# Kernel tuning notes

Measured on AMD Instinct MI355X. Metric: run time of the kernel, lower is better.

## Reference

```python
import jax, jax.numpy as jnp
import numpy as np

B, S, D = 1, 2048, 2048
H = 16
HD = D // H           # 128
FFN_H = 5632          # int(2*4*D/3) rounded up to multiple of 256
EPS = 1e-5
ROPE_THETA = 10000.0


def rms_norm(x, w, eps=EPS):
    # x * rsqrt(mean(x^2, -1) + eps) * w
    return x * jax.lax.rsqrt(jnp.mean(x * x, axis=-1, keepdims=True) + eps) * w


def apply_rope(x, cos, sin):
    # x: [B, S, H, HD]; cos/sin: [S, HD//2]
    b, s, h, hd = x.shape
    xr = x.reshape(b, s, h, hd // 2, 2)
    x_re, x_im = xr[..., 0], xr[..., 1]
    c = cos[None, :, None, :]
    sn = sin[None, :, None, :]
    o_re = x_re * c - x_im * sn
    o_im = x_re * sn + x_im * c
    return jnp.stack([o_re, o_im], axis=-1).reshape(b, s, h, hd)


def setup_inputs() -> dict:
    key = jax.random.key(0)
    ks = jax.random.split(key, 10)
    x = jax.random.normal(ks[0], (B, S, D), dtype=jnp.float32)
    # RoPE frequencies (Llama-style)
    inv_freq = 1.0 / (ROPE_THETA ** (np.arange(0, HD, 2, dtype=np.float32) / HD))
    angles = np.outer(np.arange(S, dtype=np.float32), inv_freq)  # [S, HD//2]
    freqs_cos = jnp.asarray(np.cos(angles), dtype=jnp.float32)
    freqs_sin = jnp.asarray(np.sin(angles), dtype=jnp.float32)
    # causal mask: 1 = keep, 0 = masked
    mask = jnp.tril(jnp.ones((S, S), dtype=jnp.int32))[None, None]
    sc = 0.02
    return {
        "x": x,
        "freqs_cos": freqs_cos,
        "freqs_sin": freqs_sin,
        "mask": mask,
        "wq": jax.random.normal(ks[1], (D, D), jnp.float32) * sc,
        "wk": jax.random.normal(ks[2], (D, D), jnp.float32) * sc,
        "wv": jax.random.normal(ks[3], (D, D), jnp.float32) * sc,
        "wo": jax.random.normal(ks[4], (D, D), jnp.float32) * sc,
        "w1": jax.random.normal(ks[5], (D, FFN_H), jnp.float32) * sc,
        "w2": jax.random.normal(ks[6], (FFN_H, D), jnp.float32) * sc,
        "w3": jax.random.normal(ks[7], (D, FFN_H), jnp.float32) * sc,
        "attn_norm_w": jnp.ones((D,), jnp.float32),
        "ffn_norm_w": jnp.ones((D,), jnp.float32),
    }


def reference(x, freqs_cos, freqs_sin, mask, wq, wk, wv, wo, w1, w2, w3,
              attn_norm_w, ffn_norm_w):
    b, s, d = x.shape
    # --- attention block ---
    xn = rms_norm(x, attn_norm_w)
    q = (xn @ wq).reshape(b, s, H, HD)
    k = (xn @ wk).reshape(b, s, H, HD)
    v = (xn @ wv).reshape(b, s, H, HD)
    q = apply_rope(q, freqs_cos, freqs_sin)
    k = apply_rope(k, freqs_cos, freqs_sin)
    scores = jnp.einsum('bqhd,bkhd->bhqk', q, k) / jnp.sqrt(jnp.float32(HD))
    scores = jnp.where(mask == 0, -jnp.inf, scores)
    probs = jax.nn.softmax(scores, axis=-1)
    attn = jnp.einsum('bhqk,bkhd->bqhd', probs, v).reshape(b, s, d)
    h = x + attn @ wo
    # --- SwiGLU FFN block ---
    hn = rms_norm(h, ffn_norm_w)
    ff = (jax.nn.silu(hn @ w1) * (hn @ w3)) @ w2
    return h + ff
```

## Files before the change

kernel.cpp:

```cpp
#include <hip/hip_runtime.h>
#include <hip/hip_bf16.h>

typedef __bf16 bf16x8 __attribute__((ext_vector_type(8)));
typedef float f32x4 __attribute__((ext_vector_type(4)));
typedef unsigned short u16x8 __attribute__((ext_vector_type(8)));
typedef unsigned short u16x4 __attribute__((ext_vector_type(4)));

#define DEV static __device__ __forceinline__

DEV unsigned short f2bf(float f) {
    unsigned u = __builtin_bit_cast(unsigned, f);
    u += 0x7fffu + ((u >> 16) & 1u);
    return (unsigned short)(u >> 16);
}
DEV float bf2f(unsigned short h) {
    unsigned u = ((unsigned)h) << 16;
    return __builtin_bit_cast(float, u);
}

DEV void gl2lds16(const void* g, void* l) {
    __builtin_amdgcn_global_load_lds(
        (const __attribute__((address_space(1))) void*)g,
        (__attribute__((address_space(3))) void*)l, 16, 0, 0);
}

#define WAITV(N) asm volatile("s_waitcnt vmcnt(" #N ")" ::: "memory")
#define SBAR()   asm volatile("s_barrier" ::: "memory")

#define STAGE128D(KT, BUF)                                                    \
    _Pragma("unroll")                                                         \
    for (int sl = 0; sl < 3; ++sl) {                                          \
        const unsigned short* sbase = (sl == 0)                               \
            ? A  + (size_t)bm * K                                             \
            : BT + (size_t)(bn + (sl - 1) * 128) * K;                         \
        _Pragma("unroll")                                                     \
        for (int j = 0; j < 2; ++j) {                                         \
            const unsigned short* g = sbase + (size_t)(srow + j * 64) * K     \
                                      + koff + (KT) * 64 + lc;                \
            gl2lds16(g, &lds[BUF][sl][wave * 512 + j * 4096]);                \
        }                                                                     \
    }

#define DSREAD128(BUF)                                                        \
    {                                                                         \
        const char* Ab = (const char*)&lds[BUF][0][0];                        \
        const char* Bb = (const char*)&lds[BUF][1 + (wn >> 1)][0];            \
        _Pragma("unroll")                                                     \
        for (int m4 = 0; m4 < 4; ++m4)                                        \
            _Pragma("unroll")                                                 \
            for (int kk = 0; kk < 2; ++kk)                                    \
                a_[m4][kk] = *(const bf16x8*)(Ab +                            \
                    (wm * 64 + m4 * 16 + lr) * 128 +                          \
                    ((kk * 64 + lg * 16) ^ xsw));                             \
        _Pragma("unroll")                                                     \
        for (int n2 = 0; n2 < 4; ++n2)                                        \
            _Pragma("unroll")                                                 \
            for (int kk = 0; kk < 2; ++kk)                                    \
                b_[n2][kk] = *(const bf16x8*)(Bb +                            \
                    ((wn & 1) * 64 + n2 * 16 + lr) * 128 +                    \
                    ((kk * 64 + lg * 16) ^ xsw));                             \
    }

#define MFMA128                                                               \
    __builtin_amdgcn_s_setprio(1);                                            \
    _Pragma("unroll")                                                         \
    for (int m4 = 0; m4 < 4; ++m4)                                            \
        _Pragma("unroll")                                                     \
        for (int n2 = 0; n2 < 4; ++n2)                                        \
            _Pragma("unroll")                                                 \
            for (int kk = 0; kk < 2; ++kk)                                    \
                acc[m4][n2] = __builtin_amdgcn_mfma_f32_16x16x32_bf16(        \
                    a_[m4][kk], b_[n2][kk], acc[m4][n2], 0, 0, 0);            \
    __builtin_amdgcn_s_setprio(0);

template <int EPI>
__global__ __launch_bounds__(512, 2)
void gemm128d(const unsigned short* __restrict__ A,
              const unsigned short* __restrict__ BT,
              unsigned short* __restrict__ outB,
              float* __restrict__ outP,
              int M, int N, int K,
              const float* __restrict__ cs, const float* __restrict__ sn,
              unsigned short* __restrict__ vT)
{
    __shared__ alignas(16) unsigned short lds[3][3][8192];
    const int tid  = threadIdx.x;
    const int lane = tid & 63;
    const int wave = tid >> 6;
    const int wm = wave >> 2;
    const int wn = wave & 3;
    const int lr = lane & 15;
    const int lg = lane >> 4;
    const int gy  = gridDim.y;
    const int lin = blockIdx.y * gridDim.x + blockIdx.x;
    const int cpx = (gridDim.x * gy) >> 3;
    const int swz = (lin & 7) * cpx + (lin >> 3);
    const int bm = (swz % gy) * 128;
    const int bn = (swz / gy) * 256;
    const int xsw  = (lr & 7) << 4;
    const int srow = tid >> 3;
    const int lc   = ((tid & 7) ^ (srow & 7)) * 8;
    int koff, NT;
    if constexpr (EPI == 1 || EPI == 3) {
        const int Kh = K >> 1; koff = blockIdx.z * Kh; NT = Kh >> 6;
    } else {
        koff = 0; NT = K >> 6;
    }

    f32x4 acc[4][4] = {};
    bf16x8 a_[4][2], b_[4][2];

    STAGE128D(0, 0);
    STAGE128D(1, 1);
    WAITV(6); SBAR();
    DSREAD128(0);

    int bc = 0;
    for (int kt = 0; kt < NT - 2; ++kt) {
        const int nb = (bc == 0) ? 2 : bc - 1;
        STAGE128D(kt + 2, nb);
        MFMA128;
        WAITV(6); SBAR();
        const int rb = (bc == 2) ? 0 : bc + 1;
        DSREAD128(rb);
        bc = rb;
    }
    MFMA128;
    WAITV(0); SBAR();
    {
        const int rb = (bc == 2) ? 0 : bc + 1;
        DSREAD128(rb);
    }
    MFMA128;

#pragma unroll
    for (int m4 = 0; m4 < 4; ++m4) {
        const int row = bm + wm * 64 + m4 * 16 + lg * 4;
#pragma unroll
        for (int n2 = 0; n2 < 4; ++n2) {
            const int col = bn + wn * 64 + n2 * 16 + lr;
            if constexpr (EPI == 4) {
                if (bn >= 4096) {
                    u16x4 o;
#pragma unroll
                    for (int r = 0; r < 4; ++r) o[r] = f2bf(acc[m4][n2][r]);
                    *(u16x4*)(vT + (size_t)(col - 4096) * 2048 + row) = o;
                } else {
#pragma unroll
                    for (int r = 0; r < 4; ++r) {
                        const float v  = acc[m4][n2][r];
                        const float vo = __shfl_xor(v, 1);
                        const int rr = row + r;
                        const int i0 = (col & 127) >> 1;
                        const float c = cs[rr * 64 + i0];
                        const float s = sn[rr * 64 + i0];
                        const float o = (lr & 1) ? (vo * s + v * c)
                                                 : (v * c - vo * s);
                        outB[(size_t)rr * N + col] = f2bf(o);
                    }
                }
            } else {
#pragma unroll
                for (int r = 0; r < 4; ++r) {
                    if constexpr (EPI == 1) {
                        outP[(size_t)blockIdx.z * M * N + (size_t)(row + r) * N + col] = acc[m4][n2][r];
                    } else if constexpr (EPI == 3) {
                        unsafeAtomicAdd(&outP[(size_t)(row + r) * N + col], acc[m4][n2][r]);
                    } else {
                        const float v  = acc[m4][n2][r];
                        const float vo = __shfl_xor(v, 1);
                        const float x1 = (lr & 1) ? vo : v;
                        const float x3 = (lr & 1) ? v : vo;
                        const float g  = x1 / (1.0f + __expf(-x1)) * x3;
                        if (!(lr & 1))
                            outB[(size_t)(row + r) * (N >> 1) + (col >> 1)] = f2bf(g);
                    }
                }
            }
        }
    }
}

__global__ __launch_bounds__(256)
void reduce2_norm(const float* __restrict__ res, const float* __restrict__ p,
                  const float* __restrict__ w, float* __restrict__ hout,
                  unsigned short* __restrict__ nout)
{
    const int row = blockIdx.x, tid = threadIdx.x;
    const float4* r4 = (const float4*)(res + (size_t)row * 2048);
    const float4* a4 = (const float4*)(p   + (size_t)row * 2048);
    const float4* b4 = (const float4*)(p + (size_t)2048 * 2048 + (size_t)row * 2048);
    float4* h4 = (float4*)(hout + (size_t)row * 2048);
    float4 h[2];
    float ss = 0.f;
#pragma unroll
    for (int i = 0; i < 2; ++i) {
        const int idx = i * 256 + tid;
        const float4 r = r4[idx], a = a4[idx], b = b4[idx];
        float4 v = make_float4(r.x + a.x + b.x, r.y + a.y + b.y,
                               r.z + a.z + b.z, r.w + a.w + b.w);
        h[i] = v; h4[idx] = v;
        ss += v.x * v.x + v.y * v.y + v.z * v.z + v.w * v.w;
    }
#pragma unroll
    for (int off = 32; off; off >>= 1) ss += __shfl_xor(ss, off);
    __shared__ float red[4];
    if ((tid & 63) == 0) red[tid >> 6] = ss;
    __syncthreads();
    const float tot = red[0] + red[1] + red[2] + red[3];
    const float sc = rsqrtf(tot * (1.0f / 2048.0f) + 1e-5f);
#pragma unroll
    for (int i = 0; i < 2; ++i) {
        const int idx = i * 256 + tid;
        const float4 wv = ((const float4*)w)[idx];
        u16x4 o;
        o[0] = f2bf(h[i].x * sc * wv.x); o[1] = f2bf(h[i].y * sc * wv.y);
        o[2] = f2bf(h[i].z * sc * wv.z); o[3] = f2bf(h[i].w * sc * wv.w);
        *(u16x4*)(nout + (size_t)row * 2048 + idx * 4) = o;
    }
}

__global__ __launch_bounds__(256)
void rmsnorm_kernel(const float* __restrict__ x, const float* __restrict__ w,
                    unsigned short* __restrict__ out)
{
    const int row = blockIdx.x;
    const int tid = threadIdx.x;
    const float* xr = x + (size_t)row * 2048;
    const float4 a = *reinterpret_cast<const float4*>(xr + tid * 8);
    const float4 b = *reinterpret_cast<const float4*>(xr + tid * 8 + 4);
    float ss = a.x * a.x + a.y * a.y + a.z * a.z + a.w * a.w
             + b.x * b.x + b.y * b.y + b.z * b.z + b.w * b.w;
#pragma unroll
    for (int off = 32; off; off >>= 1) ss += __shfl_xor(ss, off);
    __shared__ float red[4];
    if ((tid & 63) == 0) red[tid >> 6] = ss;
    __syncthreads();
    const float tot = red[0] + red[1] + red[2] + red[3];
    const float sc = rsqrtf(tot * (1.0f / 2048.0f) + 1e-5f);
    const float4 wa = *reinterpret_cast<const float4*>(w + tid * 8);
    const float4 wb = *reinterpret_cast<const float4*>(w + tid * 8 + 4);
    u16x8 o;
    o[0] = f2bf(a.x * sc * wa.x); o[1] = f2bf(a.y * sc * wa.y);
    o[2] = f2bf(a.z * sc * wa.z); o[3] = f2bf(a.w * sc * wa.w);
    o[4] = f2bf(b.x * sc * wb.x); o[5] = f2bf(b.y * sc * wb.y);
    o[6] = f2bf(b.z * sc * wb.z); o[7] = f2bf(b.w * sc * wb.w);
    *reinterpret_cast<u16x8*>(out + (size_t)row * 2048 + tid * 8) = o;
}

DEV void convT_body(const float* __restrict__ w, unsigned short* __restrict__ wT,
                    int K, int N, int rmul, int radd, int bk, int bn, int tid)
{
    __shared__ unsigned short t[64][66];
    const int r = tid >> 4, c4 = (tid & 15) * 4;
#pragma unroll
    for (int i = 0; i < 4; ++i) {
        const int row = r + i * 16;
        const float4 v = *reinterpret_cast<const float4*>(w + (size_t)(bk + row) * N + bn + c4);
        t[row][c4 + 0] = f2bf(v.x); t[row][c4 + 1] = f2bf(v.y);
        t[row][c4 + 2] = f2bf(v.z); t[row][c4 + 3] = f2bf(v.w);
    }
    __syncthreads();
#pragma unroll
    for (int i = 0; i < 4; ++i) {
        const int n = r + i * 16;
        u16x4 o;
#pragma unroll
        for (int e = 0; e < 4; ++e) o[e] = t[c4 + e][n];
        *reinterpret_cast<u16x4*>(wT + (size_t)(rmul * (bn + n) + radd) * K + bk + c4) = o;
    }
}

__global__ __launch_bounds__(256)
void convT_kernel(const float* __restrict__ w, unsigned short* __restrict__ wT,
                  int K, int N)
{
    convT_body(w, wT, K, N, 1, 0, blockIdx.y * 64, blockIdx.x * 64, threadIdx.x);
}

__global__ __launch_bounds__(256)
void convT4_kernel(const float* __restrict__ w0, const float* __restrict__ w1,
                   const float* __restrict__ w2, const float* __restrict__ w3,
                   unsigned short* __restrict__ wT)
{
    const int z = blockIdx.z;
    const float* w = (z == 0) ? w0 : (z == 1) ? w1 : (z == 2) ? w2 : w3;
    convT_body(w, wT + (size_t)z * 2048 * 2048, 2048, 2048, 1, 0,
               blockIdx.y * 64, blockIdx.x * 64, threadIdx.x);
}

__global__ __launch_bounds__(256)
void convTpair_kernel(const float* __restrict__ wa, const float* __restrict__ wb,
                      unsigned short* __restrict__ wT)
{
    const int z = blockIdx.z;
    convT_body(z ? wb : wa, wT, 2048, 5632, 2, z,
               blockIdx.y * 64, blockIdx.x * 64, threadIdx.x);
}

__global__ __launch_bounds__(512)
void flash_attn(const unsigned short* __restrict__ q,
                const unsigned short* __restrict__ k,
                const unsigned short* __restrict__ vT,
                unsigned short* __restrict__ attn)
{
    __shared__ alignas(16) unsigned short Ks[2][64][136];
    __shared__ alignas(16) unsigned short Vs[2][128][72];
    __shared__ alignas(16) unsigned short Ps[8][16][72];

    const int hh = blockIdx.y;
    const int pi = blockIdx.x;
    const int tid = threadIdx.x;
    const int lane = tid & 63, wave = tid >> 6;
    const int qt = (wave >> 2) ? (31 - pi) : pi;
    const int lr = lane & 15, lg = lane >> 4;
    const int q0 = qt * 64 + (wave & 3) * 16;
    const int myNT = qt + 1;
    const int NT   = 32 - pi;

    const int kr0 = tid >> 4, kc0 = (tid & 15) * 8;
    const int vr0 = tid >> 3, vc0 = (tid & 7) * 8;

    bf16x8 qf[4];
#pragma unroll
    for (int c = 0; c < 4; ++c)
        qf[c] = *reinterpret_cast<const bf16x8*>(
            q + (size_t)(q0 + lr) * 6144 + hh * 128 + c * 32 + lg * 8);

    f32x4 oacc[8] = {};
    float m_r[4], l_r[4];
#pragma unroll
    for (int r = 0; r < 4; ++r) { m_r[r] = -INFINITY; l_r[r] = 0.0f; }
    const float scale = 0.08838834764831845f;

    u16x8 kreg0, kreg1, vreg0, vreg1;
    auto gload = [&](int kt) {
        const int kv0 = kt * 64;
        kreg0 = *reinterpret_cast<const u16x8*>(k + (size_t)(kv0 + kr0) * 6144 + hh * 128 + kc0);
        kreg1 = *reinterpret_cast<const u16x8*>(k + (size_t)(kv0 + kr0 + 32) * 6144 + hh * 128 + kc0);
        vreg0 = *reinterpret_cast<const u16x8*>(vT + (size_t)(hh * 128 + vr0) * 2048 + kv0 + vc0);
        vreg1 = *reinterpret_cast<const u16x8*>(vT + (size_t)(hh * 128 + vr0 + 64) * 2048 + kv0 + vc0);
    };
    auto lwrite = [&](int buf) {
        *reinterpret_cast<u16x8*>(&Ks[buf][kr0][kc0])      = kreg0;
        *reinterpret_cast<u16x8*>(&Ks[buf][kr0 + 32][kc0]) = kreg1;
        *reinterpret_cast<u16x8*>(&Vs[buf][vr0][vc0])      = vreg0;
        *reinterpret_cast<u16x8*>(&Vs[buf][vr0 + 64][vc0]) = vreg1;
    };

    gload(0); lwrite(0);
    __syncthreads();

    for (int kt = 0; kt < NT; ++kt) {
        const int buf = kt & 1;
        if (kt + 1 < NT) gload(kt + 1);

        if (kt < myNT) {
            const int kv0 = kt * 64;
            const bool masked = (kt == myNT - 1);
            f32x4 s[4] = {};
            __builtin_amdgcn_s_setprio(1);
#pragma unroll
            for (int ct = 0; ct < 4; ++ct)
#pragma unroll
                for (int c = 0; c < 4; ++c) {
                    const bf16x8 kf = *reinterpret_cast<const bf16x8*>(
                        &Ks[buf][ct * 16 + lr][c * 32 + lg * 8]);
                    s[ct] = __builtin_amdgcn_mfma_f32_16x16x32_bf16(qf[c], kf, s[ct], 0, 0, 0);
                }
            __builtin_amdgcn_s_setprio(0);
#pragma unroll
            for (int ct = 0; ct < 4; ++ct)
#pragma unroll
                for (int r = 0; r < 4; ++r) {
                    float v = s[ct][r] * scale;
                    if (masked) {
                        const int kvg = kv0 + ct * 16 + lr;
                        const int qg  = q0 + lg * 4 + r;
                        if (kvg > qg) v = -INFINITY;
                    }
                    s[ct][r] = v;
                }
            float mn[4], alpha[4], rs[4];
#pragma unroll
            for (int r = 0; r < 4; ++r) {
                float v = fmaxf(fmaxf(s[0][r], s[1][r]), fmaxf(s[2][r], s[3][r]));
                v = fmaxf(v, __shfl_xor(v, 1));
                v = fmaxf(v, __shfl_xor(v, 2));
                v = fmaxf(v, __shfl_xor(v, 4));
                v = fmaxf(v, __shfl_xor(v, 8));
                mn[r] = fmaxf(m_r[r], v);
                alpha[r] = __expf(m_r[r] - mn[r]);
                m_r[r] = mn[r];
                rs[r] = 0.0f;
            }
#pragma unroll
            for (int ct = 0; ct < 4; ++ct)
#pragma unroll
                for (int r = 0; r < 4; ++r) {
                    const float p = __expf(s[ct][r] - mn[r]);
                    s[ct][r] = p;
                    rs[r] += p;
                }
#pragma unroll
            for (int r = 0; r < 4; ++r) {
                float t2 = rs[r];
                t2 += __shfl_xor(t2, 1);
                t2 += __shfl_xor(t2, 2);
                t2 += __shfl_xor(t2, 4);
                t2 += __shfl_xor(t2, 8);
                l_r[r] = l_r[r] * alpha[r] + t2;
            }
#pragma unroll
            for (int ot = 0; ot < 8; ++ot)
#pragma unroll
                for (int r = 0; r < 4; ++r) oacc[ot][r] *= alpha[r];

#pragma unroll
            for (int ct = 0; ct < 4; ++ct)
#pragma unroll
                for (int r = 0; r < 4; ++r)
                    Ps[wave][lg * 4 + r][ct * 16 + lr] = f2bf(s[ct][r]);

            __builtin_amdgcn_s_setprio(1);
#pragma unroll
            for (int c2 = 0; c2 < 2; ++c2) {
                const bf16x8 pf = *reinterpret_cast<const bf16x8*>(
                    &Ps[wave][lr][c2 * 32 + lg * 8]);
#pragma unroll
                for (int ot = 0; ot < 8; ++ot) {
                    const bf16x8 vf = *reinterpret_cast<const bf16x8*>(
                        &Vs[buf][ot * 16 + lr][c2 * 32 + lg * 8]);
                    oacc[ot] = __builtin_amdgcn_mfma_f32_16x16x32_bf16(pf, vf, oacc[ot], 0, 0, 0);
                }
            }
            __builtin_amdgcn_s_setprio(0);
        }

        if (kt + 1 < NT) lwrite(buf ^ 1);
        __syncthreads();
    }

#pragma unroll
    for (int ot = 0; ot < 8; ++ot)
#pragma unroll
        for (int r = 0; r < 4; ++r) {
            const float v = oacc[ot][r] / l_r[r];
            attn[(size_t)(q0 + lg * 4 + r) * 2048 + hh * 128 + ot * 16 + lr] = f2bf(v);
        }
}

extern "C" void kernel_launch(void* const* d_in, const int* in_sizes, int n_in,
                              void* d_out, int out_size, void* d_ws, size_t ws_size,
                              hipStream_t stream)
{
    const float* x    = (const float*)d_in[0];
    const float* fcos = (const float*)d_in[1];
    const float* fsin = (const float*)d_in[2];
    const float* wq  = (const float*)d_in[4];
    const float* wk  = (const float*)d_in[5];
    const float* wv  = (const float*)d_in[6];
    const float* wo  = (const float*)d_in[7];
    const float* w1  = (const float*)d_in[8];
    const float* w2  = (const float*)d_in[9];
    const float* w3  = (const float*)d_in[10];
    const float* anw = (const float*)d_in[11];
    const float* fnw = (const float*)d_in[12];
    float* out = (float*)d_out;

    char* ws = (char*)d_ws;
    size_t off = 0;
    auto alloc = [&](size_t bytes) { void* p = ws + off; off += bytes; return p; };
    const size_t SZ_DD = (size_t)2048 * 2048 * 2;
    const size_t SZ_DF = (size_t)2048 * 5632 * 2;

    unsigned short* qkvoT = (unsigned short*)alloc(4 * SZ_DD);
    unsigned short* w13T  = (unsigned short*)alloc(2 * SZ_DF);
    unsigned short* w2T   = (unsigned short*)alloc(SZ_DF);

    char* reg1 = (char*)alloc((size_t)48 * 1024 * 1024);
    unsigned short* xn   = (unsigned short*)reg1;
    unsigned short* qkv  = (unsigned short*)(reg1 + SZ_DD);
    unsigned short* vTb  = (unsigned short*)(reg1 + SZ_DD + 3 * SZ_DD);
    unsigned short* ab   = (unsigned short*)(reg1 + SZ_DD + 4 * SZ_DD);
    float*          pk   = (float*)reg1;
    unsigned short* hn   = (unsigned short*)(reg1 + 4 * SZ_DD);

    char* reg2 = (char*)alloc(SZ_DF);
    unsigned short* t1 = (unsigned short*)reg2;

    convT4_kernel<<<dim3(32, 32, 4), 256, 0, stream>>>(wq, wk, wv, wo, qkvoT);
    convTpair_kernel<<<dim3(88, 32, 2), 256, 0, stream>>>(w1, w3, w13T);
    convT_kernel<<<dim3(32, 88), 256, 0, stream>>>(w2, w2T, 5632, 2048);

    rmsnorm_kernel<<<2048, 256, 0, stream>>>(x, anw, xn);
    gemm128d<4><<<dim3(24, 16), 512, 0, stream>>>(xn, qkvoT, qkv, nullptr,
                                                  2048, 6144, 2048, fcos, fsin, vTb);
    flash_attn<<<dim3(16, 16), 512, 0, stream>>>(qkv, qkv + 2048, vTb, ab);
    gemm128d<1><<<dim3(8, 16, 2), 512, 0, stream>>>(ab, qkvoT + 3 * (size_t)2048 * 2048,
                                                    nullptr, pk, 2048, 2048, 2048,
                                                    nullptr, nullptr, nullptr);
    reduce2_norm<<<2048, 256, 0, stream>>>(x, pk, fnw, out, hn);

    gemm128d<2><<<dim3(44, 16), 512, 0, stream>>>(hn, w13T, t1, nullptr,
                                                  2048, 11264, 2048,
                                                  nullptr, nullptr, nullptr);
    gemm128d<3><<<dim3(8, 16, 2), 512, 0, stream>>>(t1, w2T, nullptr, out,
                                                    2048, 2048, 5632,
                                                    nullptr, nullptr, nullptr);
}
```

Measured before the change: 432.2 us.

## Fold wo/w1/w3/w2 weight conversion into flash-attention launch as extra blocks

Only the wq/wk/wv transposes stay in front of the QKV GEMM. The wo, w1/w3 and w2 fp32-to-bf16 transposes now run as extra blocks (256 and up) in the flash attention launch, each 512-thread block doing two 64x64 tiles. Attention uses only 256 blocks, so the conversion work can fill otherwise idle CUs and overlap with attention instead of running serially. The cost is a larger LDS footprint per block, which may lower attention occupancy, and the scheduler may mix or order conversion blocks poorly alongside the attention blocks.

```diff
diff --git a/kernel.cpp b/kernel.cpp
--- a/kernel.cpp
+++ b/kernel.cpp
@@ -248,10 +248,10 @@
     *reinterpret_cast<u16x8*>(out + (size_t)row * 2048 + tid * 8) = o;
 }
 
-DEV void convT_body(const float* __restrict__ w, unsigned short* __restrict__ wT,
-                    int K, int N, int rmul, int radd, int bk, int bn, int tid)
-{
-    __shared__ unsigned short t[64][66];
+DEV void convT_half(const float* __restrict__ w, unsigned short* __restrict__ wT,
+                    int K, int N, int rmul, int radd, int bk, int bn,
+                    int tid, unsigned short (*t)[66])
+{
     const int r = tid >> 4, c4 = (tid & 15) * 4;
 #pragma unroll
     for (int i = 0; i < 4; ++i) {
@@ -272,45 +272,58 @@
 }
 
 __global__ __launch_bounds__(256)
-void convT_kernel(const float* __restrict__ w, unsigned short* __restrict__ wT,
-                  int K, int N)
-{
-    convT_body(w, wT, K, N, 1, 0, blockIdx.y * 64, blockIdx.x * 64, threadIdx.x);
-}
-
-__global__ __launch_bounds__(256)
-void convT4_kernel(const float* __restrict__ w0, const float* __restrict__ w1,
-                   const float* __restrict__ w2, const float* __restrict__ w3,
-                   unsigned short* __restrict__ wT)
-{
+void convT3_kernel(const float* __restrict__ w0, const float* __restrict__ w1,
+                   const float* __restrict__ w2v, unsigned short* __restrict__ wT)
+{
+    __shared__ unsigned short t[64][66];
     const int z = blockIdx.z;
-    const float* w = (z == 0) ? w0 : (z == 1) ? w1 : (z == 2) ? w2 : w3;
-    convT_body(w, wT + (size_t)z * 2048 * 2048, 2048, 2048, 1, 0,
-               blockIdx.y * 64, blockIdx.x * 64, threadIdx.x);
-}
-
-__global__ __launch_bounds__(256)
-void convTpair_kernel(const float* __restrict__ wa, const float* __restrict__ wb,
-                      unsigned short* __restrict__ wT)
-{
-    const int z = blockIdx.z;
-    convT_body(z ? wb : wa, wT, 2048, 5632, 2, z,
-               blockIdx.y * 64, blockIdx.x * 64, threadIdx.x);
+    const float* w = (z == 0) ? w0 : (z == 1) ? w1 : w2v;
+    convT_half(w, wT + (size_t)z * 2048 * 2048, 2048, 2048, 1, 0,
+               blockIdx.y * 64, blockIdx.x * 64, threadIdx.x, t);
 }
 
 __global__ __launch_bounds__(512)
-void flash_attn(const unsigned short* __restrict__ q,
+void flash_mega(const unsigned short* __restrict__ q,
                 const unsigned short* __restrict__ k,
                 const unsigned short* __restrict__ vT,
-                unsigned short* __restrict__ attn)
+                unsigned short* __restrict__ attn,
+                const float* __restrict__ wo, const float* __restrict__ w1,
+                const float* __restrict__ w3, const float* __restrict__ w2,
+                unsigned short* __restrict__ woT,
+                unsigned short* __restrict__ w13T,
+                unsigned short* __restrict__ w2T)
 {
     __shared__ alignas(16) unsigned short Ks[2][64][136];
     __shared__ alignas(16) unsigned short Vs[2][128][72];
     __shared__ alignas(16) unsigned short Ps[8][16][72];
-
-    const int hh = blockIdx.y;
-    const int pi = blockIdx.x;
+    __shared__ unsigned short tbuf[2][64][66];
+
+    const int bid = blockIdx.x;
     const int tid = threadIdx.x;
+
+    if (bid >= 256) {
+        const int half = tid >> 8;
+        const int t256 = tid & 255;
+        if (bid < 768) {
+            const int t2 = (bid - 256) * 2 + half;
+            convT_half(wo, woT, 2048, 2048, 1, 0,
+                       (t2 >> 5) * 64, (t2 & 31) * 64, t256, tbuf[half]);
+        } else if (bid < 3584) {
+            const int t2 = (bid - 768) * 2 + half;
+            const int z  = t2 / 2816;
+            const int rm = t2 % 2816;
+            convT_half(z ? w3 : w1, w13T, 2048, 5632, 2, z,
+                       (rm / 88) * 64, (rm % 88) * 64, t256, tbuf[half]);
+        } else {
+            const int t2 = (bid - 3584) * 2 + half;
+            convT_half(w2, w2T, 5632, 2048, 1, 0,
+                       (t2 / 32) * 64, (t2 % 32) * 64, t256, tbuf[half]);
+        }
+        return;
+    }
+
+    const int hh = bid >> 4;
+    const int pi = bid & 15;
     const int lane = tid & 63, wave = tid >> 6;
     const int qt = (wave >> 2) ? (31 - pi) : pi;
     const int lr = lane & 15, lg = lane >> 4;
@@ -489,14 +502,14 @@
     char* reg2 = (char*)alloc(SZ_DF);
     unsigned short* t1 = (unsigned short*)reg2;
 
-    convT4_kernel<<<dim3(32, 32, 4), 256, 0, stream>>>(wq, wk, wv, wo, qkvoT);
-    convTpair_kernel<<<dim3(88, 32, 2), 256, 0, stream>>>(w1, w3, w13T);
-    convT_kernel<<<dim3(32, 88), 256, 0, stream>>>(w2, w2T, 5632, 2048);
+    convT3_kernel<<<dim3(32, 32, 3), 256, 0, stream>>>(wq, wk, wv, qkvoT);
 
     rmsnorm_kernel<<<2048, 256, 0, stream>>>(x, anw, xn);
     gemm128d<4><<<dim3(24, 16), 512, 0, stream>>>(xn, qkvoT, qkv, nullptr,
                                                   2048, 6144, 2048, fcos, fsin, vTb);
-    flash_attn<<<dim3(16, 16), 512, 0, stream>>>(qkv, qkv + 2048, vTb, ab);
+    flash_mega<<<4992, 512, 0, stream>>>(qkv, qkv + 2048, vTb, ab,
+                                         wo, w1, w3, w2,
+                                         qkvoT + 3 * (size_t)2048 * 2048, w13T, w2T);
     gemm128d<1><<<dim3(8, 16, 2), 512, 0, stream>>>(ab, qkvoT + 3 * (size_t)2048 * 2048,
                                                     nullptr, pk, 2048, 2048, 2048,
                                                     nullptr, nullptr, nullptr);
```

After: 423.9 us. About the same (-1.9%).
